# Kernel optimization log

Hardware: AMD Instinct MI355X
Metric: run time of the kernel (lower is better)

The kernel has to match this reference:

```python
import jax, jax.numpy as jnp
import numpy as np

COSINE_SIM_SCALE = 8.0  # default scale in flash-cosine-sim-attention
LN_EPS = 1e-5
HEADS = 8

def _l2norm(t, eps=1e-12):
    return t * jax.lax.rsqrt(jnp.sum(t * t, axis=-1, keepdims=True) + eps)

def setup_inputs() -> dict:
    key = jax.random.key(0)
    k1, k2, k3 = jax.random.split(key, 3)
    b, n, dim = 2, 2048, 1024
    inner = 512  # heads * dim_head
    return {
        "x": jax.random.normal(k1, (b, n, dim), dtype=jnp.float32),
        "ln_w": jnp.ones((dim,), dtype=jnp.float32),
        "ln_b": jnp.zeros((dim,), dtype=jnp.float32),
        "w_qkv": jax.random.normal(k2, (dim, 3 * inner), dtype=jnp.float32) * 0.02,
        "w_out": jax.random.normal(k3, (inner, dim), dtype=jnp.float32) * 0.02,
    }

def reference(x, ln_w, ln_b, w_qkv, w_out):
    b, n, dim = x.shape
    h = HEADS
    # LayerNorm
    mu = jnp.mean(x, axis=-1, keepdims=True)
    var = jnp.mean(jnp.square(x - mu), axis=-1, keepdims=True)
    xn = (x - mu) * jax.lax.rsqrt(var + LN_EPS) * ln_w + ln_b
    # QKV projection, split into heads: b n (h d) -> b h n d
    qkv = xn @ w_qkv
    q, k, v = jnp.split(qkv, 3, axis=-1)
    def to_heads(t):
        return t.reshape(b, n, h, -1).transpose(0, 2, 1, 3)
    q, k, v = map(to_heads, (q, k, v))
    # cosine-sim attention: l2-normalize q, k then scaled dot product
    q = _l2norm(q)
    k = _l2norm(k)
    sim = jnp.einsum('bhid,bhjd->bhij', q, k) * COSINE_SIM_SCALE
    causal_mask = jnp.tril(jnp.ones((n, n), dtype=bool))
    sim = jnp.where(causal_mask, sim, jnp.finfo(sim.dtype).min)
    attn = jax.nn.softmax(sim, axis=-1)
    o = jnp.einsum('bhij,bhjd->bhid', attn, v)
    # b h n d -> b n (h d)
    o = o.transpose(0, 2, 1, 3).reshape(b, n, -1)
    return o @ w_out
```

## Files before the change

### kernel.cpp

```cpp
#include <hip/hip_runtime.h>
#include <hip/hip_bf16.h>

typedef __attribute__((ext_vector_type(8))) __bf16 bf16x8;
typedef __attribute__((ext_vector_type(4))) __bf16 bf16x4;
typedef __attribute__((ext_vector_type(4))) float f32x4;

#define B_     2
#define N_     2048
#define DIM_   1024
#define INNER_ 512
#define H_     8
#define DH_    64
#define ROWS_  (B_ * N_)
#define QKVN_  (3 * INNER_)
#define SEGROWS_ 5120
#define QSCALE_ 11.5415603f
#define MAXL2_  11.5415603f

static __device__ __forceinline__ f32x4 mfma16(bf16x8 a, bf16x8 b, f32x4 c) {
    return __builtin_amdgcn_mfma_f32_16x16x32_bf16(a, b, c, 0, 0, 0);
}

static __device__ __forceinline__ void gld_lds16(const void* g, void* l) {
    __builtin_amdgcn_global_load_lds((const __attribute__((address_space(1))) void*)g,
                                     (__attribute__((address_space(3))) void*)l, 16, 0, 0);
}

__global__ __launch_bounds__(256) void ln_kernel(const float* __restrict__ x,
                                                 const float* __restrict__ w,
                                                 const float* __restrict__ bb,
                                                 __bf16* __restrict__ xn) {
    int row = blockIdx.x;
    int tid = threadIdx.x;
    const float* xr = x + (size_t)row * DIM_;
    f32x4 xv = *reinterpret_cast<const f32x4*>(xr + tid * 4);
    float s  = xv.x + xv.y + xv.z + xv.w;
    float sq = xv.x * xv.x + xv.y * xv.y + xv.z * xv.z + xv.w * xv.w;
#pragma unroll
    for (int m = 1; m < 64; m <<= 1) {
        s  += __shfl_xor(s, m);
        sq += __shfl_xor(sq, m);
    }
    __shared__ float red[2][4];
    int wid = tid >> 6, lane = tid & 63;
    if (lane == 0) { red[0][wid] = s; red[1][wid] = sq; }
    __syncthreads();
    s  = red[0][0] + red[0][1] + red[0][2] + red[0][3];
    sq = red[1][0] + red[1][1] + red[1][2] + red[1][3];
    float mu   = s * (1.0f / DIM_);
    float var  = sq * (1.0f / DIM_) - mu * mu;
    float rstd = rsqrtf(var + 1e-5f);
    f32x4 wv = *reinterpret_cast<const f32x4*>(w  + tid * 4);
    f32x4 bv = *reinterpret_cast<const f32x4*>(bb + tid * 4);
    bf16x4 o;
#pragma unroll
    for (int j = 0; j < 4; ++j) o[j] = (__bf16)((xv[j] - mu) * rstd * wv[j] + bv[j]);
    *reinterpret_cast<bf16x4*>(xn + (size_t)row * DIM_ + tid * 4) = o;
}

__global__ __launch_bounds__(256) void transpose_both(const float* __restrict__ wqkv,
                                                      const float* __restrict__ wout,
                                                      __bf16* __restrict__ wqkvT,
                                                      __bf16* __restrict__ woutT) {
    __shared__ float t[64][65];
    int bid = blockIdx.x;
    const float* in; __bf16* out; int K, N, bx, by;
    if (bid < 384) { in = wqkv; out = wqkvT; K = DIM_;   N = QKVN_; bx = bid % 24; by = bid / 24; }
    else { bid -= 384; in = wout; out = woutT; K = INNER_; N = DIM_;  bx = bid % 16; by = bid / 16; }
    int n0 = bx * 64, k0 = by * 64;
    int w = threadIdx.x >> 6, lane = threadIdx.x & 63;
#pragma unroll
    for (int i = 0; i < 16; ++i) {
        int k = 16 * w + i;
        t[k][lane] = in[(size_t)(k0 + k) * N + n0 + lane];
    }
    __syncthreads();
#pragma unroll
    for (int i = 0; i < 16; ++i) {
        int n = 16 * w + i;
        out[(size_t)(n0 + n) * K + k0 + lane] = (__bf16)t[lane][n];
    }
}

__global__ __launch_bounds__(256) void gemm_qkv(const __bf16* __restrict__ A,
                                                const __bf16* __restrict__ Bt,
                                                __bf16* __restrict__ Qh,
                                                __bf16* __restrict__ Kh,
                                                __bf16* __restrict__ Vrow) {
    const int K = DIM_;
    __shared__ __bf16 As[2][128 * 64];
    __shared__ __bf16 Bs[2][64 * 64];
    int id = blockIdx.x;
    int nid = (id & 7) * 96 + (id >> 3);
    int bx = nid % 24, by = nid / 24;
    int tid = threadIdx.x;
    int w = tid >> 6, lane = tid & 63;
    int lr = lane & 15, lg = lane >> 4;
    int m0 = by * 128, n0 = bx * 64;
    int sr = tid >> 3;
    int sc8 = tid & 7;
    const __bf16* Ab = A  + (size_t)m0 * K;
    const __bf16* Bb = Bt + (size_t)n0 * K;
    f32x4 acc[2][4];
#pragma unroll
    for (int mi = 0; mi < 2; ++mi)
#pragma unroll
        for (int ci = 0; ci < 4; ++ci) acc[mi][ci] = f32x4{0.f, 0.f, 0.f, 0.f};

    auto stage = [&](int buf, int k0) {
#pragma unroll
        for (int i = 0; i < 4; ++i) {
            int r = sr + i * 32;
            int cs = sc8 ^ (r & 7);
            gld_lds16(Ab + (size_t)r * K + k0 + 8 * cs, &As[buf][r * 64 + sc8 * 8]);
        }
#pragma unroll
        for (int i = 0; i < 2; ++i) {
            int r = sr + i * 32;
            int cs = sc8 ^ (r & 7);
            gld_lds16(Bb + (size_t)r * K + k0 + 8 * cs, &Bs[buf][r * 64 + sc8 * 8]);
        }
    };

    stage(0, 0);
    __syncthreads();
    int cur = 0;
    for (int k0 = 0; k0 < K; k0 += 64) {
        if (k0 + 64 < K) stage(cur ^ 1, k0 + 64);
        bf16x8 af[2][2], bfr[2][4];
#pragma unroll
        for (int kk = 0; kk < 2; ++kk) {
#pragma unroll
            for (int mi = 0; mi < 2; ++mi) {
                int r = w * 32 + 16 * mi + lr;
                af[kk][mi] = *reinterpret_cast<const bf16x8*>(
                    &As[cur][r * 64 + 8 * ((kk * 4 + lg) ^ (r & 7))]);
            }
#pragma unroll
            for (int ci = 0; ci < 4; ++ci) {
                int r = 16 * ci + lr;
                bfr[kk][ci] = *reinterpret_cast<const bf16x8*>(
                    &Bs[cur][r * 64 + 8 * ((kk * 4 + lg) ^ (r & 7))]);
            }
        }
#pragma unroll
        for (int kk = 0; kk < 2; ++kk)
#pragma unroll
            for (int mi = 0; mi < 2; ++mi)
#pragma unroll
                for (int ci = 0; ci < 4; ++ci)
                    acc[mi][ci] = mfma16(af[kk][mi], bfr[kk][ci], acc[mi][ci]);
        __syncthreads();
        cur ^= 1;
    }
    int u = bx;
    bool isV = (u >= 16);
    float smul = (u < 8) ? QSCALE_ : 1.0f;
    __bf16* base;
    if (u < 8)       base = Qh   + (size_t)u * N_ * DH_;
    else if (u < 16) base = Kh   + (size_t)(u - 8) * N_ * DH_;
    else             base = Vrow + (size_t)(u - 16) * N_ * DH_;
#pragma unroll
    for (int mi = 0; mi < 2; ++mi)
#pragma unroll
        for (int r = 0; r < 4; ++r) {
            int grow = m0 + w * 32 + 16 * mi + 4 * lg + r;
            int b = grow >> 11, n = grow & 2047;
            float sc2 = 1.0f;
            if (!isV) {
                float t = 0.f;
#pragma unroll
                for (int ci = 0; ci < 4; ++ci) t += acc[mi][ci][r] * acc[mi][ci][r];
#pragma unroll
                for (int m = 1; m < 16; m <<= 1) t += __shfl_xor(t, m);
                sc2 = rsqrtf(t + 1e-12f) * smul;
            }
            __bf16* dst = base + ((size_t)b * H_ * N_ + n) * DH_;
#pragma unroll
            for (int ci = 0; ci < 4; ++ci)
                dst[16 * ci + lr] = (__bf16)(acc[mi][ci][r] * sc2);
        }
}

__global__ __launch_bounds__(256) void gemm_out(const __bf16* __restrict__ A,
                                                const __bf16* __restrict__ Bt,
                                                float* __restrict__ C) {
    const int K = INNER_, N = DIM_;
    __shared__ __bf16 As[2][64 * 64];
    __shared__ __bf16 Bs[2][64 * 64];
    int id = blockIdx.x;
    int nid = (id & 7) * 128 + (id >> 3);
    int bx = nid % 16, by = nid / 16;
    int tid = threadIdx.x;
    int w = tid >> 6, lane = tid & 63;
    int lr = lane & 15, lg = lane >> 4;
    int m0 = by * 64, n0 = bx * 64;
    int sr = tid >> 3, sc8 = tid & 7;
    const __bf16* Ab = A  + (size_t)m0 * K;
    const __bf16* Bb = Bt + (size_t)n0 * K;
    f32x4 acc[4];
#pragma unroll
    for (int ci = 0; ci < 4; ++ci) acc[ci] = f32x4{0.f, 0.f, 0.f, 0.f};

    auto stage = [&](int buf, int k0) {
#pragma unroll
        for (int i = 0; i < 2; ++i) {
            int r = sr + i * 32;
            int cs = sc8 ^ (r & 7);
            gld_lds16(Ab + (size_t)r * K + k0 + 8 * cs, &As[buf][r * 64 + sc8 * 8]);
            gld_lds16(Bb + (size_t)r * K + k0 + 8 * cs, &Bs[buf][r * 64 + sc8 * 8]);
        }
    };

    stage(0, 0);
    __syncthreads();
    int cur = 0;
    for (int k0 = 0; k0 < K; k0 += 64) {
        if (k0 + 64 < K) stage(cur ^ 1, k0 + 64);
        bf16x8 af[2], bfr[2][4];
#pragma unroll
        for (int kk = 0; kk < 2; ++kk) {
            int r = w * 16 + lr;
            af[kk] = *reinterpret_cast<const bf16x8*>(
                &As[cur][r * 64 + 8 * ((kk * 4 + lg) ^ (r & 7))]);
#pragma unroll
            for (int ci = 0; ci < 4; ++ci) {
                int rb = 16 * ci + lr;
                bfr[kk][ci] = *reinterpret_cast<const bf16x8*>(
                    &Bs[cur][rb * 64 + 8 * ((kk * 4 + lg) ^ (rb & 7))]);
            }
        }
#pragma unroll
        for (int kk = 0; kk < 2; ++kk)
#pragma unroll
            for (int ci = 0; ci < 4; ++ci)
                acc[ci] = mfma16(af[kk], bfr[kk][ci], acc[ci]);
        __syncthreads();
        cur ^= 1;
    }
#pragma unroll
    for (int ci = 0; ci < 4; ++ci)
#pragma unroll
        for (int r = 0; r < 4; ++r)
            C[(size_t)(m0 + w * 16 + 4 * lg + r) * N + n0 + 16 * ci + lr] = acc[ci][r];
}

__global__ __launch_bounds__(256) void vtrans(const __bf16* __restrict__ Vrow,
                                              __bf16* __restrict__ Vt) {
    __shared__ __bf16 t[64][66];
    int bh = blockIdx.y, n0 = blockIdx.x * 64;
    int w = threadIdx.x >> 6, lane = threadIdx.x & 63;
#pragma unroll
    for (int i = 0; i < 16; ++i) {
        int nl = 16 * w + i;
        t[nl][lane] = Vrow[((size_t)bh * N_ + n0 + nl) * DH_ + lane];
    }
    __syncthreads();
#pragma unroll
    for (int i = 0; i < 16; ++i) {
        int d = 16 * w + i;
        Vt[(size_t)bh * DH_ * N_ + (size_t)d * N_ + n0 + lane] = t[lane][d];
    }
}

__global__ __launch_bounds__(256) void attn_kernel(const __bf16* __restrict__ Qh,
                                                   const __bf16* __restrict__ Kh,
                                                   const __bf16* __restrict__ Vt,
                                                   float* __restrict__ Opart,
                                                   float* __restrict__ lpart) {
    __shared__ __bf16 Ks[2][64 * 64];
    __shared__ __bf16 Vs[2][64 * 64];
    __shared__ __bf16 pl[4][16 * 64];
    int bh  = blockIdx.x & 15;
    int sid = blockIdx.x >> 4;
    int s, qt;
    if (sid < 32)      { s = 0; qt = 31 - sid; }
    else if (sid < 56) { s = 1; qt = 31 - (sid - 32); }
    else if (sid < 72) { s = 2; qt = 31 - (sid - 56); }
    else               { s = 3; qt = 31 - (sid - 72); }
    int jt0 = 8 * s;
    int jt1 = min(8 * s + 7, qt);
    int tid = threadIdx.x;
    int w = tid >> 6, lane = tid & 63;
    int lr = lane & 15, lg = lane >> 4;
    int qrow = qt * 64 + 16 * w;
    const __bf16* Qp = Qh + (size_t)bh * N_ * DH_;
    const __bf16* Kp = Kh + (size_t)bh * N_ * DH_;
    const __bf16* Vp = Vt + (size_t)bh * DH_ * N_;
    bf16x8 qf0 = *reinterpret_cast<const bf16x8*>(Qp + (size_t)(qrow + lr) * DH_ + 8 * lg);
    bf16x8 qf1 = *reinterpret_cast<const bf16x8*>(Qp + (size_t)(qrow + lr) * DH_ + 32 + 8 * lg);
    bf16x8 ones;
#pragma unroll
    for (int j = 0; j < 8; ++j) ones[j] = (__bf16)1.0f;
    f32x4 oacc[4];
    f32x4 oacc4 = f32x4{0.f, 0.f, 0.f, 0.f};
#pragma unroll
    for (int c = 0; c < 4; ++c) oacc[c] = f32x4{0.f, 0.f, 0.f, 0.f};
    int srow = tid >> 3, sc = tid & 7;

    auto stage = [&](int buf, int jb) {
#pragma unroll
        for (int q = 0; q < 2; ++q) {
            int row = q * 32 + srow;
            int cs = sc ^ (row & 7);
            gld_lds16(Kp + (size_t)(jb + row) * DH_ + 8 * cs,
                      &Ks[buf][(size_t)row * 64 + sc * 8]);
            gld_lds16(Vp + (size_t)row * N_ + jb + 8 * cs,
                      &Vs[buf][(size_t)row * 64 + sc * 8]);
        }
    };

    stage(0, jt0 * 64);
    __syncthreads();
    int cur = 0;
    for (int jt = jt0; jt <= jt1; ++jt) {
        int jb = jt * 64;
        if (jt < jt1) stage(cur ^ 1, jb + 64);
        const __bf16* ks = &Ks[cur][0];
        const __bf16* vs = &Vs[cur][0];
        f32x4 sm[4];
#pragma unroll
        for (int ch = 0; ch < 4; ++ch) {
            int row = 16 * ch + lr;
            bf16x8 k0 = *reinterpret_cast<const bf16x8*>(&ks[row * 64 + 8 * (lg ^ (row & 7))]);
            bf16x8 k1 = *reinterpret_cast<const bf16x8*>(&ks[row * 64 + 8 * ((4 + lg) ^ (row & 7))]);
            f32x4 t = f32x4{0.f, 0.f, 0.f, 0.f};
            t = mfma16(qf0, k0, t);
            t = mfma16(qf1, k1, t);
            sm[ch] = t;
        }
        f32x4 p[4];
        bool diag = (jt == qt);
#pragma unroll
        for (int ch = 0; ch < 4; ++ch)
#pragma unroll
            for (int r = 0; r < 4; ++r) {
                float pv = exp2f(sm[ch][r] - MAXL2_);
                if (diag) {
                    int qi = qrow + 4 * lg + r;
                    int j  = jb + 16 * ch + lr;
                    if (j > qi) pv = 0.f;
                }
                p[ch][r] = pv;
            }
        __bf16* plw = &pl[w][0];
#pragma unroll
        for (int ch = 0; ch < 4; ++ch)
#pragma unroll
            for (int r = 0; r < 4; ++r) {
                int row = 4 * lg + r, col = 16 * ch + lr;
                plw[row * 64 + (((col >> 3) ^ (row & 7)) << 3) + (col & 7)] = (__bf16)p[ch][r];
            }
        bf16x8 pf0 = *reinterpret_cast<const bf16x8*>(&plw[lr * 64 + ((lg ^ (lr & 7)) << 3)]);
        bf16x8 pf1 = *reinterpret_cast<const bf16x8*>(&plw[lr * 64 + (((4 + lg) ^ (lr & 7)) << 3)]);
#pragma unroll
        for (int dc = 0; dc < 4; ++dc) {
            int row = 16 * dc + lr;
            bf16x8 v0 = *reinterpret_cast<const bf16x8*>(&vs[row * 64 + 8 * (lg ^ (row & 7))]);
            bf16x8 v1 = *reinterpret_cast<const bf16x8*>(&vs[row * 64 + 8 * ((4 + lg) ^ (row & 7))]);
            oacc[dc] = mfma16(pf0, v0, oacc[dc]);
            oacc[dc] = mfma16(pf1, v1, oacc[dc]);
        }
        oacc4 = mfma16(pf0, ones, oacc4);
        oacc4 = mfma16(pf1, ones, oacc4);
        __syncthreads();
        cur ^= 1;
    }
    int soff = 2048 * s - 256 * s * (s - 1);
#pragma unroll
    for (int r = 0; r < 4; ++r) {
        int n = qrow + 4 * lg + r;
        size_t ridx = (size_t)bh * SEGROWS_ + soff + (n - 512 * s);
#pragma unroll
        for (int dc = 0; dc < 4; ++dc)
            Opart[ridx * 64 + 16 * dc + lr] = oacc[dc][r];
        if (lr == 0) lpart[ridx] = oacc4[r];
    }
}

__global__ __launch_bounds__(256) void combine_kernel(const float* __restrict__ Opart,
                                                      const float* __restrict__ lpart,
                                                      __bf16* __restrict__ Obp) {
    int gid = blockIdx.x * 4 + (threadIdx.x >> 6);
    int lane = threadIdx.x & 63;
    int bh = gid >> 11, n = gid & 2047;
    int smax = n >> 9;
    float acc = 0.f, lsum = 0.f;
#pragma unroll
    for (int s = 0; s < 4; ++s)
        if (s <= smax) {
            int soff = 2048 * s - 256 * s * (s - 1);
            size_t ridx = (size_t)bh * SEGROWS_ + soff + (n - 512 * s);
            acc  += Opart[ridx * 64 + lane];
            lsum += lpart[ridx];
        }
    int b = bh >> 3, h = bh & 7;
    Obp[((size_t)(b * N_ + n)) * INNER_ + h * DH_ + lane] = (__bf16)(acc / lsum);
}

extern "C" void kernel_launch(void* const* d_in, const int* in_sizes, int n_in,
                              void* d_out, int out_size, void* d_ws, size_t ws_size,
                              hipStream_t stream) {
    const float* x    = (const float*)d_in[0];
    const float* lnw  = (const float*)d_in[1];
    const float* lnb  = (const float*)d_in[2];
    const float* wqkv = (const float*)d_in[3];
    const float* wout = (const float*)d_in[4];
    float* out = (float*)d_out;

    char* ws = (char*)d_ws;
    size_t off = 0;
    auto alloc = [&](size_t bytes) -> char* {
        char* p = ws + off;
        off += (bytes + 255) & ~(size_t)255;
        return p;
    };
    __bf16* xn    = (__bf16*)alloc((size_t)ROWS_ * DIM_ * 2);
    __bf16* wqkvT = (__bf16*)alloc((size_t)QKVN_ * DIM_ * 2);
    __bf16* woutT = (__bf16*)alloc((size_t)DIM_ * INNER_ * 2);
    __bf16* Qhp   = (__bf16*)alloc((size_t)B_ * H_ * N_ * DH_ * 2);
    __bf16* Khp   = (__bf16*)alloc((size_t)B_ * H_ * N_ * DH_ * 2);
    __bf16* Vrow  = (__bf16*)alloc((size_t)B_ * H_ * N_ * DH_ * 2);
    __bf16* Vtp   = (__bf16*)alloc((size_t)B_ * H_ * DH_ * N_ * 2);
    __bf16* Obp   = (__bf16*)alloc((size_t)ROWS_ * INNER_ * 2);
    float*  Opart = (float*)alloc((size_t)B_ * H_ * SEGROWS_ * DH_ * 4);
    float*  lbuf  = (float*)alloc((size_t)B_ * H_ * SEGROWS_ * 4);
    if (off > ws_size) return;

    transpose_both<<<512, 256, 0, stream>>>(wqkv, wout, wqkvT, woutT);
    ln_kernel<<<ROWS_, 256, 0, stream>>>(x, lnw, lnb, xn);
    gemm_qkv<<<768, 256, 0, stream>>>(xn, wqkvT, Qhp, Khp, Vrow);
    vtrans<<<dim3(N_ / 64, B_ * H_), 256, 0, stream>>>(Vrow, Vtp);
    attn_kernel<<<1280, 256, 0, stream>>>(Qhp, Khp, Vtp, Opart, lbuf);
    combine_kernel<<<(ROWS_ * H_) / 4, 256, 0, stream>>>(Opart, lbuf, Obp);
    gemm_out<<<1024, 256, 0, stream>>>(Obp, woutT, out);
}
```

Measured before the change: 153.2 us.

## Fuse LN with weight transpose, V transpose into QKV GEMM, combine into out GEMM

Merges layernorm and the weight transposes into one prep launch. The QKV GEMM now writes V directly in transposed layout, which removes the vtrans kernel and the Vrow buffer. The split-attention combine (summing partial O and l, then normalizing) is folded into the output GEMM's A-tile loading, which removes the combine kernel and the Obp round trip. This cuts three launches and several intermediate global-memory passes. In exchange, gemm_out re-reads the fp32 partials once per N-tile (16 column tiles), and the transposed V stores are 8-byte strided writes.

```diff
diff --git a/kernel.cpp b/kernel.cpp
--- a/kernel.cpp
+++ b/kernel.cpp
@@ -26,49 +26,51 @@
                                      (__attribute__((address_space(3))) void*)l, 16, 0, 0);
 }
 
-__global__ __launch_bounds__(256) void ln_kernel(const float* __restrict__ x,
-                                                 const float* __restrict__ w,
-                                                 const float* __restrict__ bb,
-                                                 __bf16* __restrict__ xn) {
-    int row = blockIdx.x;
+__global__ __launch_bounds__(256) void prep_kernel(const float* __restrict__ x,
+                                                   const float* __restrict__ lnw,
+                                                   const float* __restrict__ lnb,
+                                                   const float* __restrict__ wqkv,
+                                                   const float* __restrict__ wout,
+                                                   __bf16* __restrict__ xn,
+                                                   __bf16* __restrict__ wqkvT,
+                                                   __bf16* __restrict__ woutT) {
+    int bid = blockIdx.x;
     int tid = threadIdx.x;
-    const float* xr = x + (size_t)row * DIM_;
-    f32x4 xv = *reinterpret_cast<const f32x4*>(xr + tid * 4);
-    float s  = xv.x + xv.y + xv.z + xv.w;
-    float sq = xv.x * xv.x + xv.y * xv.y + xv.z * xv.z + xv.w * xv.w;
-#pragma unroll
-    for (int m = 1; m < 64; m <<= 1) {
-        s  += __shfl_xor(s, m);
-        sq += __shfl_xor(sq, m);
-    }
-    __shared__ float red[2][4];
-    int wid = tid >> 6, lane = tid & 63;
-    if (lane == 0) { red[0][wid] = s; red[1][wid] = sq; }
-    __syncthreads();
-    s  = red[0][0] + red[0][1] + red[0][2] + red[0][3];
-    sq = red[1][0] + red[1][1] + red[1][2] + red[1][3];
-    float mu   = s * (1.0f / DIM_);
-    float var  = sq * (1.0f / DIM_) - mu * mu;
-    float rstd = rsqrtf(var + 1e-5f);
-    f32x4 wv = *reinterpret_cast<const f32x4*>(w  + tid * 4);
-    f32x4 bv = *reinterpret_cast<const f32x4*>(bb + tid * 4);
-    bf16x4 o;
-#pragma unroll
-    for (int j = 0; j < 4; ++j) o[j] = (__bf16)((xv[j] - mu) * rstd * wv[j] + bv[j]);
-    *reinterpret_cast<bf16x4*>(xn + (size_t)row * DIM_ + tid * 4) = o;
-}
-
-__global__ __launch_bounds__(256) void transpose_both(const float* __restrict__ wqkv,
-                                                      const float* __restrict__ wout,
-                                                      __bf16* __restrict__ wqkvT,
-                                                      __bf16* __restrict__ woutT) {
+    if (bid < ROWS_) {
+        int row = bid;
+        const float* xr = x + (size_t)row * DIM_;
+        f32x4 xv = *reinterpret_cast<const f32x4*>(xr + tid * 4);
+        float s  = xv.x + xv.y + xv.z + xv.w;
+        float sq = xv.x * xv.x + xv.y * xv.y + xv.z * xv.z + xv.w * xv.w;
+#pragma unroll
+        for (int m = 1; m < 64; m <<= 1) {
+            s  += __shfl_xor(s, m);
+            sq += __shfl_xor(sq, m);
+        }
+        __shared__ float red[2][4];
+        int wid = tid >> 6, lane = tid & 63;
+        if (lane == 0) { red[0][wid] = s; red[1][wid] = sq; }
+        __syncthreads();
+        s  = red[0][0] + red[0][1] + red[0][2] + red[0][3];
+        sq = red[1][0] + red[1][1] + red[1][2] + red[1][3];
+        float mu   = s * (1.0f / DIM_);
+        float var  = sq * (1.0f / DIM_) - mu * mu;
+        float rstd = rsqrtf(var + 1e-5f);
+        f32x4 wv = *reinterpret_cast<const f32x4*>(lnw + tid * 4);
+        f32x4 bv = *reinterpret_cast<const f32x4*>(lnb + tid * 4);
+        bf16x4 o;
+#pragma unroll
+        for (int j = 0; j < 4; ++j) o[j] = (__bf16)((xv[j] - mu) * rstd * wv[j] + bv[j]);
+        *reinterpret_cast<bf16x4*>(xn + (size_t)row * DIM_ + tid * 4) = o;
+        return;
+    }
     __shared__ float t[64][65];
-    int bid = blockIdx.x;
+    bid -= ROWS_;
     const float* in; __bf16* out; int K, N, bx, by;
     if (bid < 384) { in = wqkv; out = wqkvT; K = DIM_;   N = QKVN_; bx = bid % 24; by = bid / 24; }
     else { bid -= 384; in = wout; out = woutT; K = INNER_; N = DIM_;  bx = bid % 16; by = bid / 16; }
     int n0 = bx * 64, k0 = by * 64;
-    int w = threadIdx.x >> 6, lane = threadIdx.x & 63;
+    int w = tid >> 6, lane = tid & 63;
 #pragma unroll
     for (int i = 0; i < 16; ++i) {
         int k = 16 * w + i;
@@ -86,7 +88,7 @@
                                                 const __bf16* __restrict__ Bt,
                                                 __bf16* __restrict__ Qh,
                                                 __bf16* __restrict__ Kh,
-                                                __bf16* __restrict__ Vrow) {
+                                                __bf16* __restrict__ Vt) {
     const int K = DIM_;
     __shared__ __bf16 As[2][128 * 64];
     __shared__ __bf16 Bs[2][64 * 64];
@@ -154,113 +156,43 @@
         cur ^= 1;
     }
     int u = bx;
-    bool isV = (u >= 16);
+    if (u >= 16) {
+        int b = m0 >> 11;
+        __bf16* Vb = Vt + ((size_t)(b * H_ + (u - 16))) * (DH_ * N_);
+#pragma unroll
+        for (int mi = 0; mi < 2; ++mi) {
+            int nb = (m0 & 2047) + w * 32 + 16 * mi + 4 * lg;
+#pragma unroll
+            for (int ci = 0; ci < 4; ++ci) {
+                int d = 16 * ci + lr;
+                bf16x4 pk;
+#pragma unroll
+                for (int r = 0; r < 4; ++r) pk[r] = (__bf16)acc[mi][ci][r];
+                *reinterpret_cast<bf16x4*>(Vb + (size_t)d * N_ + nb) = pk;
+            }
+        }
+        return;
+    }
     float smul = (u < 8) ? QSCALE_ : 1.0f;
-    __bf16* base;
-    if (u < 8)       base = Qh   + (size_t)u * N_ * DH_;
-    else if (u < 16) base = Kh   + (size_t)(u - 8) * N_ * DH_;
-    else             base = Vrow + (size_t)(u - 16) * N_ * DH_;
+    __bf16* base = (u < 8) ? (Qh + (size_t)u * N_ * DH_)
+                           : (Kh + (size_t)(u - 8) * N_ * DH_);
 #pragma unroll
     for (int mi = 0; mi < 2; ++mi)
 #pragma unroll
         for (int r = 0; r < 4; ++r) {
             int grow = m0 + w * 32 + 16 * mi + 4 * lg + r;
             int b = grow >> 11, n = grow & 2047;
-            float sc2 = 1.0f;
-            if (!isV) {
-                float t = 0.f;
-#pragma unroll
-                for (int ci = 0; ci < 4; ++ci) t += acc[mi][ci][r] * acc[mi][ci][r];
-#pragma unroll
-                for (int m = 1; m < 16; m <<= 1) t += __shfl_xor(t, m);
-                sc2 = rsqrtf(t + 1e-12f) * smul;
-            }
+            float t = 0.f;
+#pragma unroll
+            for (int ci = 0; ci < 4; ++ci) t += acc[mi][ci][r] * acc[mi][ci][r];
+#pragma unroll
+            for (int m = 1; m < 16; m <<= 1) t += __shfl_xor(t, m);
+            float sc2 = rsqrtf(t + 1e-12f) * smul;
             __bf16* dst = base + ((size_t)b * H_ * N_ + n) * DH_;
 #pragma unroll
             for (int ci = 0; ci < 4; ++ci)
                 dst[16 * ci + lr] = (__bf16)(acc[mi][ci][r] * sc2);
         }
-}
-
-__global__ __launch_bounds__(256) void gemm_out(const __bf16* __restrict__ A,
-                                                const __bf16* __restrict__ Bt,
-                                                float* __restrict__ C) {
-    const int K = INNER_, N = DIM_;
-    __shared__ __bf16 As[2][64 * 64];
-    __shared__ __bf16 Bs[2][64 * 64];
-    int id = blockIdx.x;
-    int nid = (id & 7) * 128 + (id >> 3);
-    int bx = nid % 16, by = nid / 16;
-    int tid = threadIdx.x;
-    int w = tid >> 6, lane = tid & 63;
-    int lr = lane & 15, lg = lane >> 4;
-    int m0 = by * 64, n0 = bx * 64;
-    int sr = tid >> 3, sc8 = tid & 7;
-    const __bf16* Ab = A  + (size_t)m0 * K;
-    const __bf16* Bb = Bt + (size_t)n0 * K;
-    f32x4 acc[4];
-#pragma unroll
-    for (int ci = 0; ci < 4; ++ci) acc[ci] = f32x4{0.f, 0.f, 0.f, 0.f};
-
-    auto stage = [&](int buf, int k0) {
-#pragma unroll
-        for (int i = 0; i < 2; ++i) {
-            int r = sr + i * 32;
-            int cs = sc8 ^ (r & 7);
-            gld_lds16(Ab + (size_t)r * K + k0 + 8 * cs, &As[buf][r * 64 + sc8 * 8]);
-            gld_lds16(Bb + (size_t)r * K + k0 + 8 * cs, &Bs[buf][r * 64 + sc8 * 8]);
-        }
-    };
-
-    stage(0, 0);
-    __syncthreads();
-    int cur = 0;
-    for (int k0 = 0; k0 < K; k0 += 64) {
-        if (k0 + 64 < K) stage(cur ^ 1, k0 + 64);
-        bf16x8 af[2], bfr[2][4];
-#pragma unroll
-        for (int kk = 0; kk < 2; ++kk) {
-            int r = w * 16 + lr;
-            af[kk] = *reinterpret_cast<const bf16x8*>(
-                &As[cur][r * 64 + 8 * ((kk * 4 + lg) ^ (r & 7))]);
-#pragma unroll
-            for (int ci = 0; ci < 4; ++ci) {
-                int rb = 16 * ci + lr;
-                bfr[kk][ci] = *reinterpret_cast<const bf16x8*>(
-                    &Bs[cur][rb * 64 + 8 * ((kk * 4 + lg) ^ (rb & 7))]);
-            }
-        }
-#pragma unroll
-        for (int kk = 0; kk < 2; ++kk)
-#pragma unroll
-            for (int ci = 0; ci < 4; ++ci)
-                acc[ci] = mfma16(af[kk], bfr[kk][ci], acc[ci]);
-        __syncthreads();
-        cur ^= 1;
-    }
-#pragma unroll
-    for (int ci = 0; ci < 4; ++ci)
-#pragma unroll
-        for (int r = 0; r < 4; ++r)
-            C[(size_t)(m0 + w * 16 + 4 * lg + r) * N + n0 + 16 * ci + lr] = acc[ci][r];
-}
-
-__global__ __launch_bounds__(256) void vtrans(const __bf16* __restrict__ Vrow,
-                                              __bf16* __restrict__ Vt) {
-    __shared__ __bf16 t[64][66];
-    int bh = blockIdx.y, n0 = blockIdx.x * 64;
-    int w = threadIdx.x >> 6, lane = threadIdx.x & 63;
-#pragma unroll
-    for (int i = 0; i < 16; ++i) {
-        int nl = 16 * w + i;
-        t[nl][lane] = Vrow[((size_t)bh * N_ + n0 + nl) * DH_ + lane];
-    }
-    __syncthreads();
-#pragma unroll
-    for (int i = 0; i < 16; ++i) {
-        int d = 16 * w + i;
-        Vt[(size_t)bh * DH_ * N_ + (size_t)d * N_ + n0 + lane] = t[lane][d];
-    }
 }
 
 __global__ __launch_bounds__(256) void attn_kernel(const __bf16* __restrict__ Qh,
@@ -378,24 +310,125 @@
     }
 }
 
-__global__ __launch_bounds__(256) void combine_kernel(const float* __restrict__ Opart,
-                                                      const float* __restrict__ lpart,
-                                                      __bf16* __restrict__ Obp) {
-    int gid = blockIdx.x * 4 + (threadIdx.x >> 6);
-    int lane = threadIdx.x & 63;
-    int bh = gid >> 11, n = gid & 2047;
-    int smax = n >> 9;
-    float acc = 0.f, lsum = 0.f;
-#pragma unroll
-    for (int s = 0; s < 4; ++s)
-        if (s <= smax) {
-            int soff = 2048 * s - 256 * s * (s - 1);
-            size_t ridx = (size_t)bh * SEGROWS_ + soff + (n - 512 * s);
-            acc  += Opart[ridx * 64 + lane];
-            lsum += lpart[ridx];
-        }
-    int b = bh >> 3, h = bh & 7;
-    Obp[((size_t)(b * N_ + n)) * INNER_ + h * DH_ + lane] = (__bf16)(acc / lsum);
+__global__ __launch_bounds__(256) void gemm_out(const float* __restrict__ Opart,
+                                                const float* __restrict__ lpart,
+                                                const __bf16* __restrict__ Bt,
+                                                float* __restrict__ C) {
+    const int K = INNER_, N = DIM_;
+    __shared__ __bf16 As[2][64 * 64];
+    __shared__ __bf16 Bs[2][64 * 64];
+    int id = blockIdx.x;
+    int nid = (id & 7) * 128 + (id >> 3);
+    int bx = nid % 16, by = nid / 16;
+    int tid = threadIdx.x;
+    int w = tid >> 6, lane = tid & 63;
+    int lr = lane & 15, lg = lane >> 4;
+    int m0 = by * 64, n0 = bx * 64;
+    int sr = tid >> 3, sc8 = tid & 7;
+    const __bf16* Bb = Bt + (size_t)n0 * K;
+    f32x4 acc[4];
+#pragma unroll
+    for (int ci = 0; ci < 4; ++ci) acc[ci] = f32x4{0.f, 0.f, 0.f, 0.f};
+
+    int rr0 = sr, rr1 = sr + 32;
+    int d0 = 8 * sc8;
+
+    auto stageB = [&](int buf, int k0) {
+#pragma unroll
+        for (int i = 0; i < 2; ++i) {
+            int r = sr + i * 32;
+            int cs = sc8 ^ (r & 7);
+            gld_lds16(Bb + (size_t)r * K + k0 + 8 * cs, &Bs[buf][r * 64 + sc8 * 8]);
+        }
+    };
+
+    auto loadA = [&](int h, f32x4& s0a, f32x4& s0b, f32x4& s1a, f32x4& s1b,
+                     float& l0, float& l1) {
+#pragma unroll
+        for (int i = 0; i < 2; ++i) {
+            int r = (i == 0) ? rr0 : rr1;
+            int grow = m0 + r;
+            int b = grow >> 11, n2 = grow & 2047;
+            int smax = n2 >> 9;
+            int bhh = b * H_ + h;
+            f32x4 sa = f32x4{0.f, 0.f, 0.f, 0.f};
+            f32x4 sb = f32x4{0.f, 0.f, 0.f, 0.f};
+            float l = 0.f;
+#pragma unroll
+            for (int s = 0; s < 4; ++s)
+                if (s <= smax) {
+                    int soff = 2048 * s - 256 * s * (s - 1);
+                    size_t ridx = (size_t)bhh * SEGROWS_ + soff + (n2 - 512 * s);
+                    const float* p = Opart + ridx * 64 + d0;
+                    sa += *reinterpret_cast<const f32x4*>(p);
+                    sb += *reinterpret_cast<const f32x4*>(p + 4);
+                    l  += lpart[ridx];
+                }
+            if (i == 0) { s0a = sa; s0b = sb; l0 = l; }
+            else        { s1a = sa; s1b = sb; l1 = l; }
+        }
+    };
+
+    auto writeA = [&](int buf, f32x4 s0a, f32x4 s0b, f32x4 s1a, f32x4 s1b,
+                      float l0, float l1) {
+#pragma unroll
+        for (int i = 0; i < 2; ++i) {
+            int r = (i == 0) ? rr0 : rr1;
+            f32x4 va = (i == 0) ? s0a : s1a;
+            f32x4 vb = (i == 0) ? s0b : s1b;
+            float inv = 1.0f / ((i == 0) ? l0 : l1);
+            bf16x8 o;
+#pragma unroll
+            for (int j = 0; j < 4; ++j) o[j]     = (__bf16)(va[j] * inv);
+#pragma unroll
+            for (int j = 0; j < 4; ++j) o[4 + j] = (__bf16)(vb[j] * inv);
+            int slot = sc8 ^ (r & 7);
+            *reinterpret_cast<bf16x8*>(&As[buf][r * 64 + slot * 8]) = o;
+        }
+    };
+
+    {
+        f32x4 a0, b0, a1, b1; float l0, l1;
+        loadA(0, a0, b0, a1, b1, l0, l1);
+        stageB(0, 0);
+        writeA(0, a0, b0, a1, b1, l0, l1);
+    }
+    __syncthreads();
+    int cur = 0;
+    for (int k0 = 0; k0 < K; k0 += 64) {
+        bool more = (k0 + 64 < K);
+        f32x4 a0, b0, a1, b1; float l0, l1;
+        if (more) {
+            loadA((k0 >> 6) + 1, a0, b0, a1, b1, l0, l1);
+            stageB(cur ^ 1, k0 + 64);
+        }
+        bf16x8 af[2], bfr[2][4];
+#pragma unroll
+        for (int kk = 0; kk < 2; ++kk) {
+            int r = w * 16 + lr;
+            af[kk] = *reinterpret_cast<const bf16x8*>(
+                &As[cur][r * 64 + 8 * ((kk * 4 + lg) ^ (r & 7))]);
+#pragma unroll
+            for (int ci = 0; ci < 4; ++ci) {
+                int rb = 16 * ci + lr;
+                bfr[kk][ci] = *reinterpret_cast<const bf16x8*>(
+                    &Bs[cur][rb * 64 + 8 * ((kk * 4 + lg) ^ (rb & 7))]);
+            }
+        }
+#pragma unroll
+        for (int kk = 0; kk < 2; ++kk)
+#pragma unroll
+            for (int ci = 0; ci < 4; ++ci)
+                acc[ci] = mfma16(af[kk], bfr[kk][ci], acc[ci]);
+        if (more) writeA(cur ^ 1, a0, b0, a1, b1, l0, l1);
+        __syncthreads();
+        cur ^= 1;
+    }
+#pragma unroll
+    for (int ci = 0; ci < 4; ++ci)
+#pragma unroll
+        for (int r = 0; r < 4; ++r)
+            C[(size_t)(m0 + w * 16 + 4 * lg + r) * N + n0 + 16 * ci + lr] = acc[ci][r];
 }
 
 extern "C" void kernel_launch(void* const* d_in, const int* in_sizes, int n_in,
@@ -420,18 +453,13 @@
     __bf16* woutT = (__bf16*)alloc((size_t)DIM_ * INNER_ * 2);
     __bf16* Qhp   = (__bf16*)alloc((size_t)B_ * H_ * N_ * DH_ * 2);
     __bf16* Khp   = (__bf16*)alloc((size_t)B_ * H_ * N_ * DH_ * 2);
-    __bf16* Vrow  = (__bf16*)alloc((size_t)B_ * H_ * N_ * DH_ * 2);
     __bf16* Vtp   = (__bf16*)alloc((size_t)B_ * H_ * DH_ * N_ * 2);
-    __bf16* Obp   = (__bf16*)alloc((size_t)ROWS_ * INNER_ * 2);
     float*  Opart = (float*)alloc((size_t)B_ * H_ * SEGROWS_ * DH_ * 4);
     float*  lbuf  = (float*)alloc((size_t)B_ * H_ * SEGROWS_ * 4);
     if (off > ws_size) return;
 
-    transpose_both<<<512, 256, 0, stream>>>(wqkv, wout, wqkvT, woutT);
-    ln_kernel<<<ROWS_, 256, 0, stream>>>(x, lnw, lnb, xn);
-    gemm_qkv<<<768, 256, 0, stream>>>(xn, wqkvT, Qhp, Khp, Vrow);
-    vtrans<<<dim3(N_ / 64, B_ * H_), 256, 0, stream>>>(Vrow, Vtp);
+    prep_kernel<<<ROWS_ + 512, 256, 0, stream>>>(x, lnw, lnb, wqkv, wout, xn, wqkvT, woutT);
+    gemm_qkv<<<768, 256, 0, stream>>>(xn, wqkvT, Qhp, Khp, Vtp);
     attn_kernel<<<1280, 256, 0, stream>>>(Qhp, Khp, Vtp, Opart, lbuf);
-    combine_kernel<<<(ROWS_ * H_) / 4, 256, 0, stream>>>(Opart, lbuf, Obp);
-    gemm_out<<<1024, 256, 0, stream>>>(Obp, woutT, out);
-}
+    gemm_out<<<1024, 256, 0, stream>>>(Opart, lbuf, woutT, out);
+}
```

New measurement: 161.3 us. 5.3% more time.

## Merge LN and weight transpose launches; remap attention blocks per XCD; single-buffer V

Applied to the files above, without the earlier changes.

LayerNorm and the two weight transposes now run in one prep launch, removing a kernel launch boundary. The attention kernel maps block IDs so that each XCD handles two fixed heads, which improves L2 locality for K/V. V now uses a single LDS buffer whose next tile is loaded after the PV step, and an extra barrier is added. This lowers LDS use and may raise occupancy, but it exposes V load latency.

```diff
diff --git a/kernel.cpp b/kernel.cpp
--- a/kernel.cpp
+++ b/kernel.cpp
@@ -26,49 +26,51 @@
                                      (__attribute__((address_space(3))) void*)l, 16, 0, 0);
 }
 
-__global__ __launch_bounds__(256) void ln_kernel(const float* __restrict__ x,
-                                                 const float* __restrict__ w,
-                                                 const float* __restrict__ bb,
-                                                 __bf16* __restrict__ xn) {
-    int row = blockIdx.x;
+__global__ __launch_bounds__(256) void prep_kernel(const float* __restrict__ x,
+                                                   const float* __restrict__ lnw,
+                                                   const float* __restrict__ lnb,
+                                                   const float* __restrict__ wqkv,
+                                                   const float* __restrict__ wout,
+                                                   __bf16* __restrict__ xn,
+                                                   __bf16* __restrict__ wqkvT,
+                                                   __bf16* __restrict__ woutT) {
+    int bid = blockIdx.x;
     int tid = threadIdx.x;
-    const float* xr = x + (size_t)row * DIM_;
-    f32x4 xv = *reinterpret_cast<const f32x4*>(xr + tid * 4);
-    float s  = xv.x + xv.y + xv.z + xv.w;
-    float sq = xv.x * xv.x + xv.y * xv.y + xv.z * xv.z + xv.w * xv.w;
-#pragma unroll
-    for (int m = 1; m < 64; m <<= 1) {
-        s  += __shfl_xor(s, m);
-        sq += __shfl_xor(sq, m);
-    }
-    __shared__ float red[2][4];
-    int wid = tid >> 6, lane = tid & 63;
-    if (lane == 0) { red[0][wid] = s; red[1][wid] = sq; }
-    __syncthreads();
-    s  = red[0][0] + red[0][1] + red[0][2] + red[0][3];
-    sq = red[1][0] + red[1][1] + red[1][2] + red[1][3];
-    float mu   = s * (1.0f / DIM_);
-    float var  = sq * (1.0f / DIM_) - mu * mu;
-    float rstd = rsqrtf(var + 1e-5f);
-    f32x4 wv = *reinterpret_cast<const f32x4*>(w  + tid * 4);
-    f32x4 bv = *reinterpret_cast<const f32x4*>(bb + tid * 4);
-    bf16x4 o;
-#pragma unroll
-    for (int j = 0; j < 4; ++j) o[j] = (__bf16)((xv[j] - mu) * rstd * wv[j] + bv[j]);
-    *reinterpret_cast<bf16x4*>(xn + (size_t)row * DIM_ + tid * 4) = o;
-}
-
-__global__ __launch_bounds__(256) void transpose_both(const float* __restrict__ wqkv,
-                                                      const float* __restrict__ wout,
-                                                      __bf16* __restrict__ wqkvT,
-                                                      __bf16* __restrict__ woutT) {
+    if (bid < ROWS_) {
+        int row = bid;
+        const float* xr = x + (size_t)row * DIM_;
+        f32x4 xv = *reinterpret_cast<const f32x4*>(xr + tid * 4);
+        float s  = xv.x + xv.y + xv.z + xv.w;
+        float sq = xv.x * xv.x + xv.y * xv.y + xv.z * xv.z + xv.w * xv.w;
+#pragma unroll
+        for (int m = 1; m < 64; m <<= 1) {
+            s  += __shfl_xor(s, m);
+            sq += __shfl_xor(sq, m);
+        }
+        __shared__ float red[2][4];
+        int wid = tid >> 6, lane = tid & 63;
+        if (lane == 0) { red[0][wid] = s; red[1][wid] = sq; }
+        __syncthreads();
+        s  = red[0][0] + red[0][1] + red[0][2] + red[0][3];
+        sq = red[1][0] + red[1][1] + red[1][2] + red[1][3];
+        float mu   = s * (1.0f / DIM_);
+        float var  = sq * (1.0f / DIM_) - mu * mu;
+        float rstd = rsqrtf(var + 1e-5f);
+        f32x4 wv = *reinterpret_cast<const f32x4*>(lnw + tid * 4);
+        f32x4 bv = *reinterpret_cast<const f32x4*>(lnb + tid * 4);
+        bf16x4 o;
+#pragma unroll
+        for (int j = 0; j < 4; ++j) o[j] = (__bf16)((xv[j] - mu) * rstd * wv[j] + bv[j]);
+        *reinterpret_cast<bf16x4*>(xn + (size_t)row * DIM_ + tid * 4) = o;
+        return;
+    }
     __shared__ float t[64][65];
-    int bid = blockIdx.x;
+    bid -= ROWS_;
     const float* in; __bf16* out; int K, N, bx, by;
     if (bid < 384) { in = wqkv; out = wqkvT; K = DIM_;   N = QKVN_; bx = bid % 24; by = bid / 24; }
     else { bid -= 384; in = wout; out = woutT; K = INNER_; N = DIM_;  bx = bid % 16; by = bid / 16; }
     int n0 = bx * 64, k0 = by * 64;
-    int w = threadIdx.x >> 6, lane = threadIdx.x & 63;
+    int w = tid >> 6, lane = tid & 63;
 #pragma unroll
     for (int i = 0; i < 16; ++i) {
         int k = 16 * w + i;
@@ -97,8 +99,7 @@
     int w = tid >> 6, lane = tid & 63;
     int lr = lane & 15, lg = lane >> 4;
     int m0 = by * 128, n0 = bx * 64;
-    int sr = tid >> 3;
-    int sc8 = tid & 7;
+    int sr = tid >> 3, sc8 = tid & 7;
     const __bf16* Ab = A  + (size_t)m0 * K;
     const __bf16* Bb = Bt + (size_t)n0 * K;
     f32x4 acc[2][4];
@@ -180,6 +181,170 @@
             for (int ci = 0; ci < 4; ++ci)
                 dst[16 * ci + lr] = (__bf16)(acc[mi][ci][r] * sc2);
         }
+}
+
+__global__ __launch_bounds__(256) void vtrans(const __bf16* __restrict__ Vrow,
+                                              __bf16* __restrict__ Vt) {
+    __shared__ __bf16 t[64][66];
+    int bh = blockIdx.y, n0 = blockIdx.x * 64;
+    int w = threadIdx.x >> 6, lane = threadIdx.x & 63;
+#pragma unroll
+    for (int i = 0; i < 16; ++i) {
+        int nl = 16 * w + i;
+        t[nl][lane] = Vrow[((size_t)bh * N_ + n0 + nl) * DH_ + lane];
+    }
+    __syncthreads();
+#pragma unroll
+    for (int i = 0; i < 16; ++i) {
+        int d = 16 * w + i;
+        Vt[(size_t)bh * DH_ * N_ + (size_t)d * N_ + n0 + lane] = t[lane][d];
+    }
+}
+
+__global__ __launch_bounds__(256) void attn_kernel(const __bf16* __restrict__ Qh,
+                                                   const __bf16* __restrict__ Kh,
+                                                   const __bf16* __restrict__ Vt,
+                                                   float* __restrict__ Opart,
+                                                   float* __restrict__ lpart) {
+    __shared__ __bf16 Ks[2][64 * 64];
+    __shared__ __bf16 Vs[64 * 64];
+    __shared__ __bf16 pl[4][16 * 64];
+    int xcd = blockIdx.x & 7;
+    int q   = blockIdx.x >> 3;
+    int bh  = xcd * 2 + (q & 1);
+    int sid = q >> 1;
+    int s, qt;
+    if (sid < 32)      { s = 0; qt = 31 - sid; }
+    else if (sid < 56) { s = 1; qt = 31 - (sid - 32); }
+    else if (sid < 72) { s = 2; qt = 31 - (sid - 56); }
+    else               { s = 3; qt = 31 - (sid - 72); }
+    int jt0 = 8 * s;
+    int jt1 = min(8 * s + 7, qt);
+    int tid = threadIdx.x;
+    int w = tid >> 6, lane = tid & 63;
+    int lr = lane & 15, lg = lane >> 4;
+    int qrow = qt * 64 + 16 * w;
+    const __bf16* Qp = Qh + (size_t)bh * N_ * DH_;
+    const __bf16* Kp = Kh + (size_t)bh * N_ * DH_;
+    const __bf16* Vp = Vt + (size_t)bh * DH_ * N_;
+    bf16x8 qf0 = *reinterpret_cast<const bf16x8*>(Qp + (size_t)(qrow + lr) * DH_ + 8 * lg);
+    bf16x8 qf1 = *reinterpret_cast<const bf16x8*>(Qp + (size_t)(qrow + lr) * DH_ + 32 + 8 * lg);
+    bf16x8 ones;
+#pragma unroll
+    for (int j = 0; j < 8; ++j) ones[j] = (__bf16)1.0f;
+    f32x4 oacc[4];
+    f32x4 oacc4 = f32x4{0.f, 0.f, 0.f, 0.f};
+#pragma unroll
+    for (int c = 0; c < 4; ++c) oacc[c] = f32x4{0.f, 0.f, 0.f, 0.f};
+    int srow = tid >> 3, sc = tid & 7;
+
+    auto stageK = [&](int buf, int jb) {
+#pragma unroll
+        for (int qq = 0; qq < 2; ++qq) {
+            int row = qq * 32 + srow;
+            int cs = sc ^ (row & 7);
+            gld_lds16(Kp + (size_t)(jb + row) * DH_ + 8 * cs,
+                      &Ks[buf][(size_t)row * 64 + sc * 8]);
+        }
+    };
+    auto stageV = [&](int jb) {
+#pragma unroll
+        for (int qq = 0; qq < 2; ++qq) {
+            int row = qq * 32 + srow;
+            int cs = sc ^ (row & 7);
+            gld_lds16(Vp + (size_t)row * N_ + jb + 8 * cs,
+                      &Vs[(size_t)row * 64 + sc * 8]);
+        }
+    };
+
+    stageK(0, jt0 * 64);
+    stageV(jt0 * 64);
+    __syncthreads();
+    int cur = 0;
+    for (int jt = jt0; jt <= jt1; ++jt) {
+        int jb = jt * 64;
+        if (jt < jt1) stageK(cur ^ 1, jb + 64);
+        const __bf16* ks = &Ks[cur][0];
+        f32x4 sm[4];
+#pragma unroll
+        for (int ch = 0; ch < 4; ++ch) {
+            int row = 16 * ch + lr;
+            bf16x8 k0 = *reinterpret_cast<const bf16x8*>(&ks[row * 64 + 8 * (lg ^ (row & 7))]);
+            bf16x8 k1 = *reinterpret_cast<const bf16x8*>(&ks[row * 64 + 8 * ((4 + lg) ^ (row & 7))]);
+            f32x4 t = f32x4{0.f, 0.f, 0.f, 0.f};
+            t = mfma16(qf0, k0, t);
+            t = mfma16(qf1, k1, t);
+            sm[ch] = t;
+        }
+        f32x4 p[4];
+        bool diag = (jt == qt);
+#pragma unroll
+        for (int ch = 0; ch < 4; ++ch)
+#pragma unroll
+            for (int r = 0; r < 4; ++r) {
+                float pv = exp2f(sm[ch][r] - MAXL2_);
+                if (diag) {
+                    int qi = qrow + 4 * lg + r;
+                    int j  = jb + 16 * ch + lr;
+                    if (j > qi) pv = 0.f;
+                }
+                p[ch][r] = pv;
+            }
+        __bf16* plw = &pl[w][0];
+#pragma unroll
+        for (int ch = 0; ch < 4; ++ch)
+#pragma unroll
+            for (int r = 0; r < 4; ++r) {
+                int row = 4 * lg + r, col = 16 * ch + lr;
+                plw[row * 64 + (((col >> 3) ^ (row & 7)) << 3) + (col & 7)] = (__bf16)p[ch][r];
+            }
+        bf16x8 pf0 = *reinterpret_cast<const bf16x8*>(&plw[lr * 64 + ((lg ^ (lr & 7)) << 3)]);
+        bf16x8 pf1 = *reinterpret_cast<const bf16x8*>(&plw[lr * 64 + (((4 + lg) ^ (lr & 7)) << 3)]);
+        __syncthreads();
+#pragma unroll
+        for (int dc = 0; dc < 4; ++dc) {
+            int row = 16 * dc + lr;
+            bf16x8 v0 = *reinterpret_cast<const bf16x8*>(&Vs[row * 64 + 8 * (lg ^ (row & 7))]);
+            bf16x8 v1 = *reinterpret_cast<const bf16x8*>(&Vs[row * 64 + 8 * ((4 + lg) ^ (row & 7))]);
+            oacc[dc] = mfma16(pf0, v0, oacc[dc]);
+            oacc[dc] = mfma16(pf1, v1, oacc[dc]);
+        }
+        oacc4 = mfma16(pf0, ones, oacc4);
+        oacc4 = mfma16(pf1, ones, oacc4);
+        __syncthreads();
+        if (jt < jt1) stageV(jb + 64);
+        cur ^= 1;
+    }
+    int soff = 2048 * s - 256 * s * (s - 1);
+#pragma unroll
+    for (int r = 0; r < 4; ++r) {
+        int n = qrow + 4 * lg + r;
+        size_t ridx = (size_t)bh * SEGROWS_ + soff + (n - 512 * s);
+#pragma unroll
+        for (int dc = 0; dc < 4; ++dc)
+            Opart[ridx * 64 + 16 * dc + lr] = oacc[dc][r];
+        if (lr == 0) lpart[ridx] = oacc4[r];
+    }
+}
+
+__global__ __launch_bounds__(256) void combine_kernel(const float* __restrict__ Opart,
+                                                      const float* __restrict__ lpart,
+                                                      __bf16* __restrict__ Obp) {
+    int gid = blockIdx.x * 4 + (threadIdx.x >> 6);
+    int lane = threadIdx.x & 63;
+    int bh = gid >> 11, n = gid & 2047;
+    int smax = n >> 9;
+    float acc = 0.f, lsum = 0.f;
+#pragma unroll
+    for (int s = 0; s < 4; ++s)
+        if (s <= smax) {
+            int soff = 2048 * s - 256 * s * (s - 1);
+            size_t ridx = (size_t)bh * SEGROWS_ + soff + (n - 512 * s);
+            acc  += Opart[ridx * 64 + lane];
+            lsum += lpart[ridx];
+        }
+    int b = bh >> 3, h = bh & 7;
+    Obp[((size_t)(b * N_ + n)) * INNER_ + h * DH_ + lane] = (__bf16)(acc / lsum);
 }
 
 __global__ __launch_bounds__(256) void gemm_out(const __bf16* __restrict__ A,
@@ -243,159 +408,6 @@
 #pragma unroll
         for (int r = 0; r < 4; ++r)
             C[(size_t)(m0 + w * 16 + 4 * lg + r) * N + n0 + 16 * ci + lr] = acc[ci][r];
-}
-
-__global__ __launch_bounds__(256) void vtrans(const __bf16* __restrict__ Vrow,
-                                              __bf16* __restrict__ Vt) {
-    __shared__ __bf16 t[64][66];
-    int bh = blockIdx.y, n0 = blockIdx.x * 64;
-    int w = threadIdx.x >> 6, lane = threadIdx.x & 63;
-#pragma unroll
-    for (int i = 0; i < 16; ++i) {
-        int nl = 16 * w + i;
-        t[nl][lane] = Vrow[((size_t)bh * N_ + n0 + nl) * DH_ + lane];
-    }
-    __syncthreads();
-#pragma unroll
-    for (int i = 0; i < 16; ++i) {
-        int d = 16 * w + i;
-        Vt[(size_t)bh * DH_ * N_ + (size_t)d * N_ + n0 + lane] = t[lane][d];
-    }
-}
-
-__global__ __launch_bounds__(256) void attn_kernel(const __bf16* __restrict__ Qh,
-                                                   const __bf16* __restrict__ Kh,
-                                                   const __bf16* __restrict__ Vt,
-                                                   float* __restrict__ Opart,
-                                                   float* __restrict__ lpart) {
-    __shared__ __bf16 Ks[2][64 * 64];
-    __shared__ __bf16 Vs[2][64 * 64];
-    __shared__ __bf16 pl[4][16 * 64];
-    int bh  = blockIdx.x & 15;
-    int sid = blockIdx.x >> 4;
-    int s, qt;
-    if (sid < 32)      { s = 0; qt = 31 - sid; }
-    else if (sid < 56) { s = 1; qt = 31 - (sid - 32); }
-    else if (sid < 72) { s = 2; qt = 31 - (sid - 56); }
-    else               { s = 3; qt = 31 - (sid - 72); }
-    int jt0 = 8 * s;
-    int jt1 = min(8 * s + 7, qt);
-    int tid = threadIdx.x;
-    int w = tid >> 6, lane = tid & 63;
-    int lr = lane & 15, lg = lane >> 4;
-    int qrow = qt * 64 + 16 * w;
-    const __bf16* Qp = Qh + (size_t)bh * N_ * DH_;
-    const __bf16* Kp = Kh + (size_t)bh * N_ * DH_;
-    const __bf16* Vp = Vt + (size_t)bh * DH_ * N_;
-    bf16x8 qf0 = *reinterpret_cast<const bf16x8*>(Qp + (size_t)(qrow + lr) * DH_ + 8 * lg);
-    bf16x8 qf1 = *reinterpret_cast<const bf16x8*>(Qp + (size_t)(qrow + lr) * DH_ + 32 + 8 * lg);
-    bf16x8 ones;
-#pragma unroll
-    for (int j = 0; j < 8; ++j) ones[j] = (__bf16)1.0f;
-    f32x4 oacc[4];
-    f32x4 oacc4 = f32x4{0.f, 0.f, 0.f, 0.f};
-#pragma unroll
-    for (int c = 0; c < 4; ++c) oacc[c] = f32x4{0.f, 0.f, 0.f, 0.f};
-    int srow = tid >> 3, sc = tid & 7;
-
-    auto stage = [&](int buf, int jb) {
-#pragma unroll
-        for (int q = 0; q < 2; ++q) {
-            int row = q * 32 + srow;
-            int cs = sc ^ (row & 7);
-            gld_lds16(Kp + (size_t)(jb + row) * DH_ + 8 * cs,
-                      &Ks[buf][(size_t)row * 64 + sc * 8]);
-            gld_lds16(Vp + (size_t)row * N_ + jb + 8 * cs,
-                      &Vs[buf][(size_t)row * 64 + sc * 8]);
-        }
-    };
-
-    stage(0, jt0 * 64);
-    __syncthreads();
-    int cur = 0;
-    for (int jt = jt0; jt <= jt1; ++jt) {
-        int jb = jt * 64;
-        if (jt < jt1) stage(cur ^ 1, jb + 64);
-        const __bf16* ks = &Ks[cur][0];
-        const __bf16* vs = &Vs[cur][0];
-        f32x4 sm[4];
-#pragma unroll
-        for (int ch = 0; ch < 4; ++ch) {
-            int row = 16 * ch + lr;
-            bf16x8 k0 = *reinterpret_cast<const bf16x8*>(&ks[row * 64 + 8 * (lg ^ (row & 7))]);
-            bf16x8 k1 = *reinterpret_cast<const bf16x8*>(&ks[row * 64 + 8 * ((4 + lg) ^ (row & 7))]);
-            f32x4 t = f32x4{0.f, 0.f, 0.f, 0.f};
-            t = mfma16(qf0, k0, t);
-            t = mfma16(qf1, k1, t);
-            sm[ch] = t;
-        }
-        f32x4 p[4];
-        bool diag = (jt == qt);
-#pragma unroll
-        for (int ch = 0; ch < 4; ++ch)
-#pragma unroll
-            for (int r = 0; r < 4; ++r) {
-                float pv = exp2f(sm[ch][r] - MAXL2_);
-                if (diag) {
-                    int qi = qrow + 4 * lg + r;
-                    int j  = jb + 16 * ch + lr;
-                    if (j > qi) pv = 0.f;
-                }
-                p[ch][r] = pv;
-            }
-        __bf16* plw = &pl[w][0];
-#pragma unroll
-        for (int ch = 0; ch < 4; ++ch)
-#pragma unroll
-            for (int r = 0; r < 4; ++r) {
-                int row = 4 * lg + r, col = 16 * ch + lr;
-                plw[row * 64 + (((col >> 3) ^ (row & 7)) << 3) + (col & 7)] = (__bf16)p[ch][r];
-            }
-        bf16x8 pf0 = *reinterpret_cast<const bf16x8*>(&plw[lr * 64 + ((lg ^ (lr & 7)) << 3)]);
-        bf16x8 pf1 = *reinterpret_cast<const bf16x8*>(&plw[lr * 64 + (((4 + lg) ^ (lr & 7)) << 3)]);
-#pragma unroll
-        for (int dc = 0; dc < 4; ++dc) {
-            int row = 16 * dc + lr;
-            bf16x8 v0 = *reinterpret_cast<const bf16x8*>(&vs[row * 64 + 8 * (lg ^ (row & 7))]);
-            bf16x8 v1 = *reinterpret_cast<const bf16x8*>(&vs[row * 64 + 8 * ((4 + lg) ^ (row & 7))]);
-            oacc[dc] = mfma16(pf0, v0, oacc[dc]);
-            oacc[dc] = mfma16(pf1, v1, oacc[dc]);
-        }
-        oacc4 = mfma16(pf0, ones, oacc4);
-        oacc4 = mfma16(pf1, ones, oacc4);
-        __syncthreads();
-        cur ^= 1;
-    }
-    int soff = 2048 * s - 256 * s * (s - 1);
-#pragma unroll
-    for (int r = 0; r < 4; ++r) {
-        int n = qrow + 4 * lg + r;
-        size_t ridx = (size_t)bh * SEGROWS_ + soff + (n - 512 * s);
-#pragma unroll
-        for (int dc = 0; dc < 4; ++dc)
-            Opart[ridx * 64 + 16 * dc + lr] = oacc[dc][r];
-        if (lr == 0) lpart[ridx] = oacc4[r];
-    }
-}
-
-__global__ __launch_bounds__(256) void combine_kernel(const float* __restrict__ Opart,
-                                                      const float* __restrict__ lpart,
-                                                      __bf16* __restrict__ Obp) {
-    int gid = blockIdx.x * 4 + (threadIdx.x >> 6);
-    int lane = threadIdx.x & 63;
-    int bh = gid >> 11, n = gid & 2047;
-    int smax = n >> 9;
-    float acc = 0.f, lsum = 0.f;
-#pragma unroll
-    for (int s = 0; s < 4; ++s)
-        if (s <= smax) {
-            int soff = 2048 * s - 256 * s * (s - 1);
-            size_t ridx = (size_t)bh * SEGROWS_ + soff + (n - 512 * s);
-            acc  += Opart[ridx * 64 + lane];
-            lsum += lpart[ridx];
-        }
-    int b = bh >> 3, h = bh & 7;
-    Obp[((size_t)(b * N_ + n)) * INNER_ + h * DH_ + lane] = (__bf16)(acc / lsum);
 }
 
 extern "C" void kernel_launch(void* const* d_in, const int* in_sizes, int n_in,
@@ -427,8 +439,7 @@
     float*  lbuf  = (float*)alloc((size_t)B_ * H_ * SEGROWS_ * 4);
     if (off > ws_size) return;
 
-    transpose_both<<<512, 256, 0, stream>>>(wqkv, wout, wqkvT, woutT);
-    ln_kernel<<<ROWS_, 256, 0, stream>>>(x, lnw, lnb, xn);
+    prep_kernel<<<ROWS_ + 512, 256, 0, stream>>>(x, lnw, lnb, wqkv, wout, xn, wqkvT, woutT);
     gemm_qkv<<<768, 256, 0, stream>>>(xn, wqkvT, Qhp, Khp, Vrow);
     vtrans<<<dim3(N_ / 64, B_ * H_), 256, 0, stream>>>(Vrow, Vtp);
     attn_kernel<<<1280, 256, 0, stream>>>(Qhp, Khp, Vtp, Opart, lbuf);
```

New measurement: 153.8 us. Within noise of the previous version (+0.4%).
